# Optimization experiments

Measured on AMD Instinct MI355X. Metric: run time of the kernel, lower is better.

Reference implementation:

```python
import jax, jax.numpy as jnp
import numpy as np

S = 100        # sos_token_num
H = 12         # num heads
LY = 3         # number of residual blocks
NEG = -100.0   # attention-bias masking value


def layer_norm(x, w, b, eps=1e-5):
    u = jnp.mean(x, -1, keepdims=True)
    v = jnp.mean((x - u) ** 2, -1, keepdims=True)
    return (x - u) / jnp.sqrt(v + eps) * w + b


def quick_gelu(x):
    return x * jax.nn.sigmoid(1.702 * x)


def l2norm(x, eps=1e-12):
    return x / jnp.maximum(jnp.linalg.norm(x, axis=-1, keepdims=True), eps)


def setup_inputs() -> dict:
    key = jax.random.key(0)
    ks = iter(jax.random.split(key, 32))
    n, c, hh, ww, out_dim = 2, 768, 32, 32, 512
    r = lambda shape, s=1.0: jax.random.normal(next(ks), shape, jnp.float32) * s
    return dict(
        cls_token=r((1, n, c)),
        pix_feat=r((n, c, hh, ww)),
        last_surgery=r((1 + hh * ww, n, c)),
        attn_bias=r((n, 1, S, hh, ww)),
        qkv_w=r((LY, 3 * c, c), 0.02), qkv_b=jnp.zeros((LY, 3 * c)),
        proj_w=r((LY, c, c), 0.02), proj_b=jnp.zeros((LY, c)),
        ln1_w=jnp.ones((LY, c)), ln1_b=jnp.zeros((LY, c)),
        ln2_w=jnp.ones((LY, c)), ln2_b=jnp.zeros((LY, c)),
        fc_w=r((LY, 4 * c, c), 0.02), fc_b=jnp.zeros((LY, 4 * c)),
        fc2_w=r((LY, c, 4 * c), 0.02), fc2_b=jnp.zeros((LY, c)),
        lnp_w=jnp.ones((c,)), lnp_b=jnp.zeros((c,)),
        proj_out=r((c, out_dim), 0.02),
    )


def reference(cls_token, pix_feat, last_surgery, attn_bias,
              qkv_w, qkv_b, proj_w, proj_b,
              ln1_w, ln1_b, ln2_w, ln2_b,
              fc_w, fc_b, fc2_w, fc2_b,
              lnp_w, lnp_b, proj_out):
    n, c, hh, ww = pix_feat.shape
    L = hh * ww
    N = S + 1 + L
    d = c // H
    scale = d ** -0.5

    # ---- assemble token streams (batch-first [n, N, c]) ----
    pix_tok = pix_feat.reshape(n, c, L).transpose(2, 0, 1)          # [L, n, c]
    x = jnp.concatenate([jnp.broadcast_to(cls_token, (S, n, c)), cls_token, pix_tok], 0)
    x_sur = jnp.concatenate([jnp.broadcast_to(last_surgery[0:1], (S, n, c)), last_surgery], 0)
    xo = x.transpose(1, 0, 2)      # 'original' stream  [n, N, c]
    xs = x_sur.transpose(1, 0, 2)  # 'surgery'  stream  [n, N, c]

    # ---- build attention biases (identity downsample: bias already at (h, w)) ----
    base = jnp.zeros((N, N), jnp.float32)
    base = base.at[:, :S].set(NEG)
    base = base.at[jnp.arange(S), jnp.arange(S)].set(0.0)
    base = base.at[:S, S].set(NEG)
    plain = jnp.broadcast_to(base, (n, H, N, N))
    bias = jnp.broadcast_to(attn_bias, (n, H, S, hh, ww)).reshape(n, H, S, L)
    biased = plain.at[:, :, :S, S + 1:].set(bias)   # sos rows attend to pixels via bias

    def attention(t, l):
        # t: [n, N, c] (post-ln_1); returns (surgery_res, ori_res)
        qkv = (t @ qkv_w[l].T + qkv_b[l]).reshape(n, N, 3, H, d).transpose(2, 0, 3, 1, 4)
        q, k, v = qkv[0], qkv[1], qkv[2]   # each [n, H, N, d]
        def attend(q_, k_, mask):
            a = jax.nn.softmax(jnp.einsum('bhnd,bhmd->bhnm', q_, k_) * scale + mask, axis=-1)
            o = jnp.einsum('bhnm,bhmd->bhnd', a, v).transpose(0, 2, 1, 3).reshape(n, N, c)
            return o @ proj_w[l].T + proj_b[l]
        x_ori_res = attend(q, k, biased)   # standard pass, biased mask (attn_mask[0])
        x_res = attend(v, v, plain)        # q = k = v surgery pass (attn_mask[1])
        return x_res, x_ori_res

    for l in range(LY):
        t = layer_norm(xo, ln1_w[l], ln1_b[l])
        res_sur, res_ori = attention(t, l)
        xo = xo + res_ori
        xo = xo + (quick_gelu(layer_norm(xo, ln2_w[l], ln2_b[l]) @ fc_w[l].T + fc_b[l]) @ fc2_w[l].T + fc2_b[l])
        xs = xs + res_sur

    # ---- heads ----
    sos = l2norm(layer_norm(xo[:, :S], lnp_w, lnp_b) @ proj_out)          # [n, S, out]
    img = l2norm(layer_norm(xs[:, S:], lnp_w, lnp_b) @ proj_out)          # [n, 1+L, out]
    img = img[:, 1:, :].transpose(0, 2, 1).reshape(n, proj_out.shape[1], hh, ww)
    return sos, img
```

## Files before the change

### kernel.cpp

```cpp
#include <hip/hip_runtime.h>
#include <math.h>


constexpr int Cc = 768;
constexpr int Ss = 100;
constexpr int Hh = 12;
constexpr int Ll = 1024;
constexpr int Nn = 1125;
constexpr int NB = 2;
constexpr int VTS = 1216;
constexpr float QS = 0.18033688011112042f;
constexpr float LOG2E = 1.4426950408889634f;

typedef unsigned short u16;
typedef unsigned int u32;
typedef __attribute__((ext_vector_type(8))) short short8v;
typedef __attribute__((ext_vector_type(8))) unsigned short ushort8v;
typedef __attribute__((ext_vector_type(4))) float f32x4;
typedef __attribute__((ext_vector_type(4))) unsigned int u32x4;

__device__ inline u16 f2bf(float f) {
  unsigned u = __builtin_bit_cast(unsigned int, f);
  unsigned r = u + 0x7fffu + ((u >> 16) & 1u);
  return (u16)(r >> 16);
}
__device__ inline float bf2f(u16 v) {
  return __builtin_bit_cast(float, (unsigned int)v << 16);
}
__device__ inline unsigned cvtpk(float lo, float hi) {
  unsigned r;
  asm("v_cvt_pk_bf16_f32 %0, %1, %2" : "=v"(r) : "v"(lo), "v"(hi));
  return r;
}
__device__ inline float max3f(float a, float b, float c) {
  float r;
  asm("v_max3_f32 %0, %1, %2, %3" : "=v"(r) : "v"(a), "v"(b), "v"(c));
  return r;
}

__device__ inline int swz(int row, int col) {
  return (row << 6) + ((((col >> 3) ^ (row & 7)) << 3) | (col & 7));
}

__global__ __launch_bounds__(256) void assemble_kernel(
    const float* __restrict__ cls, const float* __restrict__ pix,
    const float* __restrict__ sur, float* __restrict__ xo, float* __restrict__ xs) {
  int idx = blockIdx.x * 256 + (int)threadIdx.x;
  int total = NB * Nn * Cc;
  if (idx >= total) return;
  int ch = idx % Cc;
  int t  = (idx / Cc) % Nn;
  int b  = idx / (Cc * Nn);
  float vo, vs;
  if (t <= Ss) vo = cls[b * Cc + ch];
  else         vo = pix[(size_t)b * Cc * Ll + (size_t)ch * Ll + (t - Ss - 1)];
  if (t < Ss)  vs = sur[b * Cc + ch];
  else         vs = sur[(size_t)(t - Ss) * NB * Cc + b * Cc + ch];
  xo[idx] = vo;
  xs[idx] = vs;
}

constexpr int CN0 = 3 * 2304 * 768;
constexpr int CN1 = 3 * 768 * 768;
constexpr int CN2 = 3 * 3072 * 768;
constexpr int CN3 = 3 * 768 * 3072;
__global__ __launch_bounds__(256) void cvt4_kernel(
    const float* __restrict__ s0, const float* __restrict__ s1,
    const float* __restrict__ s2, const float* __restrict__ s3,
    u16* __restrict__ dst) {
  int i4 = (blockIdx.x * 256 + (int)threadIdx.x) * 4;
  if (i4 >= CN0 + CN1 + CN2 + CN3) return;
  const float* src; int off;
  if (i4 < CN0)             { src = s0; off = i4; }
  else if (i4 < CN0 + CN1)  { src = s1; off = i4 - CN0; }
  else if (i4 < CN0 + CN1 + CN2) { src = s2; off = i4 - CN0 - CN1; }
  else                      { src = s3; off = i4 - CN0 - CN1 - CN2; }
  float4 v = *(const float4*)(src + off);
  *(ushort4*)(dst + i4) = make_ushort4(f2bf(v.x), f2bf(v.y), f2bf(v.z), f2bf(v.w));
}

__global__ __launch_bounds__(256) void transpose_po_kernel(
    const float* __restrict__ in, u16* __restrict__ out) {
  int id = blockIdx.x * 256 + (int)threadIdx.x;
  if (id >= 512 * 768) return;
  int nidx = id / 768, k = id - nidx * 768;
  out[id] = f2bf(in[(size_t)k * 512 + nidx]);
}

__global__ __launch_bounds__(256) void vtrans_kernel(
    const u16* __restrict__ qkv, u16* __restrict__ vtg) {
  __shared__ u16 tile[64][72];
  int tt = blockIdx.x;
  int bh = blockIdx.y;
  int b = bh / Hh, h = bh - b * Hh;
  int tid = (int)threadIdx.x;
  {
    int tl = tid >> 2, c0 = (tid & 3) << 4;
    int tok = tt * 64 + tl;
    int tokc = tok > 1124 ? 1124 : tok;
    const u16* src = qkv + ((size_t)(b * Nn + tokc)) * 2304 + 2 * Cc + h * 64 + c0;
    ushort8v v0 = *(const ushort8v*)src;
    ushort8v v1 = *(const ushort8v*)(src + 8);
    if (tok > 1124) { v0 = (ushort8v)0; v1 = (ushort8v)0; }
    *(ushort8v*)&tile[tl][c0] = v0;
    *(ushort8v*)&tile[tl][c0 + 8] = v1;
  }
  __syncthreads();
  {
    int d = tid >> 2, t0 = (tid & 3) << 4;
    ushort8v o0, o1;
#pragma unroll
    for (int j = 0; j < 8; ++j) { o0[j] = tile[t0 + j][d]; o1[j] = tile[t0 + 8 + j][d]; }
    size_t orow = ((size_t)bh * 64 + d) * VTS + tt * 64 + t0;
    *(ushort8v*)&vtg[orow] = o0;
    *(ushort8v*)&vtg[orow + 8] = o1;
  }
}

__global__ __launch_bounds__(256) void ln_kernel(
    const float* __restrict__ X, const float* __restrict__ w, const float* __restrict__ b,
    u16* __restrict__ Y, int rows_per_b, int row_off) {
  int r = blockIdx.x;
  int bb = r / rows_per_b;
  int i  = r % rows_per_b;
  const float* x = X + ((size_t)bb * Nn + row_off + i) * Cc;
  u16* y = Y + (size_t)r * Cc;
  int tid = (int)threadIdx.x;
  float v0 = x[tid], v1 = x[tid + 256], v2 = x[tid + 512];
  float s = v0 + v1 + v2;
  __shared__ float sbuf[4];
  for (int off = 32; off; off >>= 1) s += __shfl_xor(s, off);
  if ((tid & 63) == 0) sbuf[tid >> 6] = s;
  __syncthreads();
  float mean = (sbuf[0] + sbuf[1] + sbuf[2] + sbuf[3]) * (1.0f / Cc);
  float d0 = v0 - mean, d1 = v1 - mean, d2 = v2 - mean;
  float q = d0 * d0 + d1 * d1 + d2 * d2;
  __syncthreads();
  for (int off = 32; off; off >>= 1) q += __shfl_xor(q, off);
  if ((tid & 63) == 0) sbuf[tid >> 6] = q;
  __syncthreads();
  float var = (sbuf[0] + sbuf[1] + sbuf[2] + sbuf[3]) * (1.0f / Cc);
  float inv = rsqrtf(var + 1e-5f);
  y[tid]       = f2bf(d0 * inv * w[tid]       + b[tid]);
  y[tid + 256] = f2bf(d1 * inv * w[tid + 256] + b[tid + 256]);
  y[tid + 512] = f2bf(d2 * inv * w[tid + 512] + b[tid + 512]);
}

__global__ __launch_bounds__(256) void gemm64_kernel(
    const u16* __restrict__ A0, const u16* __restrict__ A1,
    const u16* __restrict__ B, const float* __restrict__ bias,
    const float* __restrict__ res0, const float* __restrict__ res1,
    float* __restrict__ outf0, float* __restrict__ outf1,
    u16* __restrict__ outb0, u16* __restrict__ outb1,
    int M, int N, int K, int act) {
  __shared__ __align__(16) u16 Als[64 * 64];
  __shared__ __align__(16) u16 Bls[128 * 64];
  int zz = blockIdx.z;
  const u16* A = zz ? A1 : A0;
  const float* res = zz ? res1 : res0;
  float* outf = zz ? outf1 : outf0;
  u16* outb = zz ? outb1 : outb0;
  int tid = (int)threadIdx.x;
  int wave = tid >> 6, lane = tid & 63, g = lane >> 4, li = lane & 15;
  int row0 = blockIdx.y * 64, col0 = blockIdx.x * 128;

  const u16* aptr[2]; int dA[2];
#pragma unroll
  for (int j = 0; j < 2; ++j) {
    int ca = tid + j * 256;
    int r = ca >> 3, c8 = ca & 7;
    dA[j] = (r << 6) + ((c8 ^ (r & 7)) << 3);
    int ra = row0 + r; if (ra > M - 1) ra = M - 1;
    aptr[j] = A + (size_t)ra * K + (c8 << 3);
  }
  const u16* bptr[4]; int dB[4];
#pragma unroll
  for (int j = 0; j < 4; ++j) {
    int cb = tid + j * 256;
    int r = cb >> 3, c8 = cb & 7;
    dB[j] = (r << 6) + ((c8 ^ (r & 7)) << 3);
    bptr[j] = B + (size_t)(col0 + r) * K + (c8 << 3);
  }

  f32x4 acc[4][2];
#pragma unroll
  for (int mi = 0; mi < 4; ++mi)
#pragma unroll
    for (int ni = 0; ni < 2; ++ni) acc[mi][ni] = (f32x4){0.f, 0.f, 0.f, 0.f};

  for (int k0 = 0; k0 < K; k0 += 64) {
    ushort8v ta[2], tb[4];
#pragma unroll
    for (int j = 0; j < 2; ++j) ta[j] = *(const ushort8v*)(aptr[j] + k0);
#pragma unroll
    for (int j = 0; j < 4; ++j) tb[j] = *(const ushort8v*)(bptr[j] + k0);
    __syncthreads();
#pragma unroll
    for (int j = 0; j < 2; ++j) *(ushort8v*)&Als[dA[j]] = ta[j];
#pragma unroll
    for (int j = 0; j < 4; ++j) *(ushort8v*)&Bls[dB[j]] = tb[j];
    __syncthreads();
#pragma unroll
    for (int kc = 0; kc < 2; ++kc) {
      short8v af[4], bfr[2];
#pragma unroll
      for (int mi = 0; mi < 4; ++mi) {
        int rr = mi * 16 + li;
        af[mi] = *(const short8v*)&Als[(rr << 6) + (((kc * 4 + g) ^ (rr & 7)) << 3)];
      }
#pragma unroll
      for (int ni = 0; ni < 2; ++ni) {
        int rb = wave * 32 + ni * 16 + li;
        bfr[ni] = *(const short8v*)&Bls[(rb << 6) + (((kc * 4 + g) ^ (rb & 7)) << 3)];
      }
      __builtin_amdgcn_s_setprio(1);
#pragma unroll
      for (int mi = 0; mi < 4; ++mi)
#pragma unroll
        for (int ni = 0; ni < 2; ++ni)
          acc[mi][ni] = __builtin_amdgcn_mfma_f32_16x16x32_bf16(af[mi], bfr[ni], acc[mi][ni], 0, 0, 0);
      __builtin_amdgcn_s_setprio(0);
    }
  }

#pragma unroll
  for (int mi = 0; mi < 4; ++mi) {
#pragma unroll
    for (int r = 0; r < 4; ++r) {
      int m = row0 + mi * 16 + g * 4 + r;
      if (m >= M) continue;
#pragma unroll
      for (int ni = 0; ni < 2; ++ni) {
        int n = col0 + wave * 32 + ni * 16 + li;
        float v = acc[mi][ni][r];
        if (bias) v += bias[n];
        if (act)  v = v / (1.0f + __expf(-1.702f * v));
        if (res)  v += res[(size_t)m * N + n];
        if (outf) outf[(size_t)m * N + n] = v;
        else      outb[(size_t)m * N + n] = f2bf(v);
      }
    }
  }
}

__global__ __launch_bounds__(256) void attn_kernel(
    const u16* __restrict__ qkv, const u16* __restrict__ vtg,
    const float* __restrict__ abias,
    u16* __restrict__ ao, u16* __restrict__ as_) {
  __shared__ __align__(16) u16 Klds[64 * 64];
  __shared__ __align__(16) u16 Vt[64 * 64];
  int id = (int)blockIdx.x;
  int virt = (id & 7) * 114 + (id >> 3);
  int gid = virt / 19;
  int qt  = virt - gid * 19;
  int z   = gid / 24;
  int bh  = gid - z * 24;
  int b = bh / Hh, h = bh - b * Hh;
  int tid = (int)threadIdx.x;
  int wave = tid >> 6, lane = tid & 63, g = lane >> 4, li = lane & 15;
  bool sosq = qt >= 17;
  u16* outp = z ? as_ : ao;

  int qbase = sosq ? (qt - 17) * 64 + wave * 16 : Ss + qt * 64 + wave * 16;
  int qtok = qbase + li;
  int qcap = sosq ? 99 : 1124;
  if (qtok > qcap) qtok = qcap;
  int qoff = z ? 2 * Cc + h * 64 : h * 64;
  int koff = z ? 2 * Cc + h * 64 : Cc + h * 64;

  short8v qf[2];
  {
    const u16* qp = qkv + ((size_t)b * Nn + qtok) * 2304 + qoff;
#pragma unroll
    for (int kc = 0; kc < 2; ++kc) {
      ushort8v a = *(const ushort8v*)(qp + kc * 32 + g * 8);
      u32x4 w;
#pragma unroll
      for (int jj = 0; jj < 4; ++jj)
        w[jj] = cvtpk(bf2f(a[2 * jj]) * QS, bf2f(a[2 * jj + 1]) * QS);
      qf[kc] = __builtin_bit_cast(short8v, w);
    }
  }

  int skey = tid >> 2;
  int sd0  = (tid & 3) << 4;
  int prow = 16 * (2 * (skey >> 5) + ((skey >> 2) & 1)) + 4 * ((skey >> 3) & 3) + (skey & 3);
  int kK0 = swz(prow, sd0), kK1 = swz(prow, sd0 + 8);
  int vI0 = swz(skey, sd0), vI1 = swz(skey, sd0 + 8);
  const u16* kbase = qkv + (size_t)b * Nn * 2304 + koff + sd0;
  const u16* vbase = vtg + ((size_t)bh * 64 + skey) * VTS + sd0;

  const int KOFF[4] = {0, 4, 32, 36};

  f32x4 oacc[4];
#pragma unroll
  for (int dt = 0; dt < 4; ++dt) oacc[dt] = (f32x4){0.f, 0.f, 0.f, 0.f};
  float mrow = -1e30f, lrow = 0.f;

  int NT = sosq ? 18 : 17;
  for (int kt = 0; kt < NT; ++kt) {
    int t0 = sosq ? (kt == 0 ? (qt - 17) * 64 : 64 * kt + 32) : 96 + 64 * kt;
    __syncthreads();
    {
      int ktok = t0 + skey; if (ktok > 1124) ktok = 1124;
      const u16* kp = kbase + (size_t)ktok * 2304;
      ushort8v k0v = *(const ushort8v*)kp;
      ushort8v k1v = *(const ushort8v*)(kp + 8);
      const u16* vp = vbase + t0;
      ushort8v v0 = *(const ushort8v*)vp;
      ushort8v v1 = *(const ushort8v*)(vp + 8);
      *(ushort8v*)&Klds[kK0] = k0v;
      *(ushort8v*)&Klds[kK1] = k1v;
      *(ushort8v*)&Vt[vI0] = v0;
      *(ushort8v*)&Vt[vI1] = v1;
    }
    __syncthreads();

    f32x4 sacc[4];
#pragma unroll
    for (int nt = 0; nt < 4; ++nt) sacc[nt] = (f32x4){0.f, 0.f, 0.f, 0.f};
    __builtin_amdgcn_s_setprio(1);
#pragma unroll
    for (int kc = 0; kc < 2; ++kc) {
#pragma unroll
      for (int nt = 0; nt < 4; ++nt) {
        short8v kb = *(const short8v*)&Klds[swz(nt * 16 + li, kc * 32 + g * 8)];
        sacc[nt] = __builtin_amdgcn_mfma_f32_16x16x32_bf16(kb, qf[kc], sacc[nt], 0, 0, 0);
      }
    }
    __builtin_amdgcn_s_setprio(0);

    int tg = t0 + 8 * g;
    if (!sosq) {
      if (kt == 0) {
#pragma unroll
        for (int nt = 0; nt < 4; ++nt)
#pragma unroll
          for (int r = 0; r < 4; ++r)
            if (tg + KOFF[nt] + r < 100) sacc[nt][r] = -1e30f;
      } else if (kt == 16) {
#pragma unroll
        for (int nt = 0; nt < 4; ++nt)
#pragma unroll
          for (int r = 0; r < 4; ++r)
            if (tg + KOFF[nt] + r > 1124) sacc[nt][r] = -1e30f;
      }
    } else {
      if (kt == 0) {
#pragma unroll
        for (int nt = 0; nt < 4; ++nt)
#pragma unroll
          for (int r = 0; r < 4; ++r)
            if (tg + KOFF[nt] + r != qtok) sacc[nt][r] = -1e30f;
      } else if (z == 0) {
        const float* bp = abias + ((size_t)b * Ss + qtok) * Ll;
#pragma unroll
        for (int nt = 0; nt < 4; ++nt)
#pragma unroll
          for (int r = 0; r < 4; ++r) {
            int tok = tg + KOFF[nt] + r;
            int bi = tok - 101; bi = bi < 0 ? 0 : bi; bi = bi > 1023 ? 1023 : bi;
            float bv = bp[bi];
            bool bad = (tok < 101) | (tok > 1124);
            sacc[nt][r] = bad ? -1e30f : fmaf(bv, LOG2E, sacc[nt][r]);
          }
      } else {
#pragma unroll
        for (int nt = 0; nt < 4; ++nt)
#pragma unroll
          for (int r = 0; r < 4; ++r) {
            int tok = tg + KOFF[nt] + r;
            if ((tok < 101) | (tok > 1124)) sacc[nt][r] = -1e30f;
          }
      }
    }

    float rmax = max3f(sacc[0][0], sacc[0][1], sacc[0][2]);
    rmax = max3f(rmax, sacc[0][3], sacc[1][0]);
    rmax = max3f(rmax, sacc[1][1], sacc[1][2]);
    rmax = max3f(rmax, sacc[1][3], sacc[2][0]);
    rmax = max3f(rmax, sacc[2][1], sacc[2][2]);
    rmax = max3f(rmax, sacc[2][3], sacc[3][0]);
    rmax = max3f(rmax, sacc[3][1], sacc[3][2]);
    rmax = fmaxf(rmax, sacc[3][3]);
    rmax = fmaxf(rmax, __shfl_xor(rmax, 16));
    rmax = fmaxf(rmax, __shfl_xor(rmax, 32));
    float mnew = fmaxf(mrow, rmax);
    float fac = __builtin_amdgcn_exp2f(mrow - mnew);
    mrow = mnew;
    float psum = 0.f;
#pragma unroll
    for (int nt = 0; nt < 4; ++nt)
#pragma unroll
      for (int r = 0; r < 4; ++r) {
        float e = __builtin_amdgcn_exp2f(sacc[nt][r] - mnew);
        sacc[nt][r] = e;
        psum += e;
      }
    psum += __shfl_xor(psum, 16);
    psum += __shfl_xor(psum, 32);
    lrow = lrow * fac + psum;
#pragma unroll
    for (int dt = 0; dt < 4; ++dt) oacc[dt] *= fac;

    __builtin_amdgcn_s_setprio(1);
#pragma unroll
    for (int kcp = 0; kcp < 2; ++kcp) {
      u32x4 pwv;
#pragma unroll
      for (int w = 0; w < 4; ++w) {
        int nt = 2 * kcp + (w >> 1);
        int r0 = (w & 1) * 2;
        pwv[w] = cvtpk(sacc[nt][r0], sacc[nt][r0 + 1]);
      }
      short8v pb = __builtin_bit_cast(short8v, pwv);
#pragma unroll
      for (int dt = 0; dt < 4; ++dt) {
        short8v va = *(const short8v*)&Vt[swz(dt * 16 + li, kcp * 32 + g * 8)];
        oacc[dt] = __builtin_amdgcn_mfma_f32_16x16x32_bf16(va, pb, oacc[dt], 0, 0, 0);
      }
    }
    __builtin_amdgcn_s_setprio(0);
  }

  int tok = qbase + li;
  if (tok <= qcap) {
    float inv = 1.0f / lrow;
    u16* op = outp + ((size_t)b * Nn + tok) * Cc + h * 64 + g * 4;
#pragma unroll
    for (int dt = 0; dt < 4; ++dt) {
      unsigned lo = cvtpk(oacc[dt][0] * inv, oacc[dt][1] * inv);
      unsigned hi = cvtpk(oacc[dt][2] * inv, oacc[dt][3] * inv);
      uint2 o2; o2.x = lo; o2.y = hi;
      *(uint2*)(op + dt * 16) = o2;
    }
  }
}

__global__ __launch_bounds__(256) void l2norm_sos_kernel(
    const float* __restrict__ Xp, float* __restrict__ out) {
  int r = blockIdx.x;
  int tid = (int)threadIdx.x;
  const float* x = Xp + (size_t)r * 512;
  float v0 = x[tid], v1 = x[tid + 256];
  float s = v0 * v0 + v1 * v1;
  __shared__ float sbuf[4];
  for (int off = 32; off; off >>= 1) s += __shfl_xor(s, off);
  if ((tid & 63) == 0) sbuf[tid >> 6] = s;
  __syncthreads();
  float tot = sbuf[0] + sbuf[1] + sbuf[2] + sbuf[3];
  float inv = 1.0f / fmaxf(sqrtf(tot), 1e-12f);
  out[(size_t)r * 512 + tid]       = v0 * inv;
  out[(size_t)r * 512 + tid + 256] = v1 * inv;
}

__global__ __launch_bounds__(256) void l2norm_img_kernel(
    const float* __restrict__ Xp, float* __restrict__ out) {
  int r = blockIdx.x;
  int b = r / 1025, ti = r % 1025;
  int tid = (int)threadIdx.x;
  const float* x = Xp + (size_t)r * 512;
  float v0 = x[tid], v1 = x[tid + 256];
  float s = v0 * v0 + v1 * v1;
  __shared__ float sbuf[4];
  for (int off = 32; off; off >>= 1) s += __shfl_xor(s, off);
  if ((tid & 63) == 0) sbuf[tid >> 6] = s;
  __syncthreads();
  float tot = sbuf[0] + sbuf[1] + sbuf[2] + sbuf[3];
  if (ti == 0) return;
  float inv = 1.0f / fmaxf(sqrtf(tot), 1e-12f);
  float* o = out + (size_t)b * 512 * 1024 + (ti - 1);
  o[(size_t)tid * 1024]         = v0 * inv;
  o[(size_t)(tid + 256) * 1024] = v1 * inv;
}

extern "C" void kernel_launch(void* const* d_in, const int* in_sizes, int n_in,
                              void* d_out, int out_size, void* d_ws, size_t ws_size,
                              hipStream_t stream) {
  const float* cls      = (const float*)d_in[0];
  const float* pix      = (const float*)d_in[1];
  const float* sur      = (const float*)d_in[2];
  const float* abias    = (const float*)d_in[3];
  const float* qkv_w    = (const float*)d_in[4];
  const float* qkv_b    = (const float*)d_in[5];
  const float* proj_w   = (const float*)d_in[6];
  const float* proj_b   = (const float*)d_in[7];
  const float* ln1_w    = (const float*)d_in[8];
  const float* ln1_b    = (const float*)d_in[9];
  const float* ln2_w    = (const float*)d_in[10];
  const float* ln2_b    = (const float*)d_in[11];
  const float* fc_w     = (const float*)d_in[12];
  const float* fc_b     = (const float*)d_in[13];
  const float* fc2_w    = (const float*)d_in[14];
  const float* fc2_b    = (const float*)d_in[15];
  const float* lnp_w    = (const float*)d_in[16];
  const float* lnp_b    = (const float*)d_in[17];
  const float* proj_o   = (const float*)d_in[18];
  float* out = (float*)d_out;

  const size_t SZ = (size_t)NB * Nn * Cc;
  float* xo      = (float*)d_ws;
  float* xs      = xo + SZ;
  float* head_pj = xs + SZ;
  u16* tln_bf = (u16*)(head_pj + 2250 * 512);
  u16* act_bf = tln_bf + (size_t)2250 * 768;
  u16* ao_bf  = act_bf + (size_t)2250 * 3072;
  u16* as_bf  = ao_bf + (size_t)2250 * 768;
  u16* wq_bf  = as_bf + (size_t)2250 * 768;
  u16* wp_bf  = wq_bf + (size_t)CN0;
  u16* wf_bf  = wp_bf + (size_t)CN1;
  u16* w2_bf  = wf_bf + (size_t)CN2;
  u16* wo_bf  = w2_bf + (size_t)CN3;
  u16* vtg    = wo_bf + (size_t)512 * 768;

  assemble_kernel<<<6750, 256, 0, stream>>>(cls, pix, sur, xo, xs);
  cvt4_kernel<<<20736, 256, 0, stream>>>(qkv_w, proj_w, fc_w, fc2_w, wq_bf);
  transpose_po_kernel<<<1536, 256, 0, stream>>>(proj_o, wo_bf);

  for (int l = 0; l < 3; ++l) {
    ln_kernel<<<2250, 256, 0, stream>>>(xo, ln1_w + l * 768, ln1_b + l * 768, tln_bf, Nn, 0);
    gemm64_kernel<<<dim3(18, 36, 1), 256, 0, stream>>>(
        tln_bf, tln_bf, wq_bf + (size_t)l * 2304 * 768, qkv_b + l * 2304,
        nullptr, nullptr, nullptr, nullptr, act_bf, act_bf, 2250, 2304, 768, 0);
    vtrans_kernel<<<dim3(19, 24), 256, 0, stream>>>(act_bf, vtg);
    attn_kernel<<<912, 256, 0, stream>>>(act_bf, vtg, abias, ao_bf, as_bf);
    gemm64_kernel<<<dim3(6, 36, 2), 256, 0, stream>>>(
        ao_bf, as_bf, wp_bf + (size_t)l * 768 * 768, proj_b + l * 768,
        xo, xs, xo, xs, nullptr, nullptr, 2250, 768, 768, 0);
    ln_kernel<<<2250, 256, 0, stream>>>(xo, ln2_w + l * 768, ln2_b + l * 768, tln_bf, Nn, 0);
    gemm64_kernel<<<dim3(24, 36, 1), 256, 0, stream>>>(
        tln_bf, tln_bf, wf_bf + (size_t)l * 3072 * 768, fc_b + l * 3072,
        nullptr, nullptr, nullptr, nullptr, act_bf, act_bf, 2250, 3072, 768, 1);
    gemm64_kernel<<<dim3(6, 36, 1), 256, 0, stream>>>(
        act_bf, act_bf, w2_bf + (size_t)l * 768 * 3072, fc2_b + l * 768,
        xo, xo, xo, xo, nullptr, nullptr, 2250, 768, 3072, 0);
  }

  ln_kernel<<<200, 256, 0, stream>>>(xo, lnp_w, lnp_b, tln_bf, 100, 0);
  ln_kernel<<<2050, 256, 0, stream>>>(xs, lnp_w, lnp_b, tln_bf + 200 * 768, 1025, 100);
  gemm64_kernel<<<dim3(4, 36, 1), 256, 0, stream>>>(
      tln_bf, tln_bf, wo_bf, nullptr,
      nullptr, nullptr, head_pj, head_pj, nullptr, nullptr, 2250, 512, 768, 0);
  l2norm_sos_kernel<<<200, 256, 0, stream>>>(head_pj, out);
  l2norm_img_kernel<<<2050, 256, 0, stream>>>(head_pj + 200 * 512, out + 102400);
}
```

Baseline: 754.8 us.

## Add 128x128 GEMM for QKV/FC and process two query fragments per attention wave

Adds a gemm128 kernel that uses 128x128 tiles with 4x4 MFMA fragments per wave, and routes the QKV and FC1 GEMMs through it. Larger tiles raise arithmetic intensity and reuse of the loaded A and B tiles. The attention kernel now handles 32 query rows per wave (128 per block) instead of 16, so each K/V tile loaded into LDS is reused across twice as many queries. The SOS query tile is restructured to cover all 100 SOS queries in one block. In exchange, register pressure goes up and the grids shrink, which can lower occupancy and leave CUs underused.

```diff
diff --git a/kernel.cpp b/kernel.cpp
--- a/kernel.cpp
+++ b/kernel.cpp
@@ -146,6 +146,89 @@
   y[tid + 512] = f2bf(d2 * inv * w[tid + 512] + b[tid + 512]);
 }
 
+__global__ __launch_bounds__(256) void gemm128_kernel(
+    const u16* __restrict__ A, const u16* __restrict__ B,
+    const float* __restrict__ bias, u16* __restrict__ outb,
+    int M, int N, int K, int act) {
+  __shared__ __align__(16) u16 Als[128 * 64];
+  __shared__ __align__(16) u16 Bls[128 * 64];
+  int tid = (int)threadIdx.x;
+  int wave = tid >> 6, lane = tid & 63, g = lane >> 4, li = lane & 15;
+  int wm = wave >> 1, wn = wave & 1;
+  int row0 = blockIdx.y * 128, col0 = blockIdx.x * 128;
+
+  const u16* aptr[4]; const u16* bptr[4]; int dsti[4];
+#pragma unroll
+  for (int j = 0; j < 4; ++j) {
+    int c = tid + j * 256;
+    int r = c >> 3, c8 = c & 7;
+    dsti[j] = (r << 6) + ((c8 ^ (r & 7)) << 3);
+    int ra = row0 + r; if (ra > M - 1) ra = M - 1;
+    aptr[j] = A + (size_t)ra * K + (c8 << 3);
+    bptr[j] = B + (size_t)(col0 + r) * K + (c8 << 3);
+  }
+
+  f32x4 acc[4][4];
+#pragma unroll
+  for (int mi = 0; mi < 4; ++mi)
+#pragma unroll
+    for (int ni = 0; ni < 4; ++ni) acc[mi][ni] = (f32x4){0.f, 0.f, 0.f, 0.f};
+
+  for (int k0 = 0; k0 < K; k0 += 64) {
+    ushort8v ta[4], tb[4];
+#pragma unroll
+    for (int j = 0; j < 4; ++j) {
+      ta[j] = *(const ushort8v*)(aptr[j] + k0);
+      tb[j] = *(const ushort8v*)(bptr[j] + k0);
+    }
+    __syncthreads();
+#pragma unroll
+    for (int j = 0; j < 4; ++j) {
+      *(ushort8v*)&Als[dsti[j]] = ta[j];
+      *(ushort8v*)&Bls[dsti[j]] = tb[j];
+    }
+    __syncthreads();
+#pragma unroll
+    for (int kc = 0; kc < 2; ++kc) {
+      short8v af[4], bfr[4];
+#pragma unroll
+      for (int mi = 0; mi < 4; ++mi) {
+        int rr = wm * 64 + mi * 16 + li;
+        af[mi] = *(const short8v*)&Als[(rr << 6) + (((kc * 4 + g) ^ (rr & 7)) << 3)];
+      }
+#pragma unroll
+      for (int ni = 0; ni < 4; ++ni) {
+        int rb = wn * 64 + ni * 16 + li;
+        bfr[ni] = *(const short8v*)&Bls[(rb << 6) + (((kc * 4 + g) ^ (rb & 7)) << 3)];
+      }
+      __builtin_amdgcn_s_setprio(1);
+#pragma unroll
+      for (int mi = 0; mi < 4; ++mi)
+#pragma unroll
+        for (int ni = 0; ni < 4; ++ni)
+          acc[mi][ni] = __builtin_amdgcn_mfma_f32_16x16x32_bf16(af[mi], bfr[ni], acc[mi][ni], 0, 0, 0);
+      __builtin_amdgcn_s_setprio(0);
+    }
+  }
+
+#pragma unroll
+  for (int mi = 0; mi < 4; ++mi) {
+#pragma unroll
+    for (int r = 0; r < 4; ++r) {
+      int m = row0 + wm * 64 + mi * 16 + g * 4 + r;
+      if (m >= M) continue;
+#pragma unroll
+      for (int ni = 0; ni < 4; ++ni) {
+        int n = col0 + wn * 64 + ni * 16 + li;
+        float v = acc[mi][ni][r];
+        if (bias) v += bias[n];
+        if (act)  v = v / (1.0f + __expf(-1.702f * v));
+        outb[(size_t)m * N + n] = f2bf(v);
+      }
+    }
+  }
+}
+
 __global__ __launch_bounds__(256) void gemm64_kernel(
     const u16* __restrict__ A0, const u16* __restrict__ A1,
     const u16* __restrict__ B, const float* __restrict__ bias,
@@ -250,27 +333,29 @@
   __shared__ __align__(16) u16 Klds[64 * 64];
   __shared__ __align__(16) u16 Vt[64 * 64];
   int id = (int)blockIdx.x;
-  int virt = (id & 7) * 114 + (id >> 3);
-  int gid = virt / 19;
-  int qt  = virt - gid * 19;
+  int virt = (id & 7) * 60 + (id >> 3);
+  int gid = virt / 10;
+  int qt  = virt - gid * 10;
   int z   = gid / 24;
   int bh  = gid - z * 24;
   int b = bh / Hh, h = bh - b * Hh;
   int tid = (int)threadIdx.x;
   int wave = tid >> 6, lane = tid & 63, g = lane >> 4, li = lane & 15;
-  bool sosq = qt >= 17;
+  bool sosq = (qt == 9);
   u16* outp = z ? as_ : ao;
 
-  int qbase = sosq ? (qt - 17) * 64 + wave * 16 : Ss + qt * 64 + wave * 16;
-  int qtok = qbase + li;
+  int qbase = sosq ? wave * 32 : 100 + qt * 128 + wave * 32;
   int qcap = sosq ? 99 : 1124;
-  if (qtok > qcap) qtok = qcap;
+  int qtokf[2];
+  qtokf[0] = qbase + li;       if (qtokf[0] > qcap) qtokf[0] = qcap;
+  qtokf[1] = qbase + 16 + li;  if (qtokf[1] > qcap) qtokf[1] = qcap;
   int qoff = z ? 2 * Cc + h * 64 : h * 64;
   int koff = z ? 2 * Cc + h * 64 : Cc + h * 64;
 
-  short8v qf[2];
-  {
-    const u16* qp = qkv + ((size_t)b * Nn + qtok) * 2304 + qoff;
+  short8v qf[2][2];
+#pragma unroll
+  for (int f = 0; f < 2; ++f) {
+    const u16* qp = qkv + ((size_t)b * Nn + qtokf[f]) * 2304 + qoff;
 #pragma unroll
     for (int kc = 0; kc < 2; ++kc) {
       ushort8v a = *(const ushort8v*)(qp + kc * 32 + g * 8);
@@ -278,7 +363,7 @@
 #pragma unroll
       for (int jj = 0; jj < 4; ++jj)
         w[jj] = cvtpk(bf2f(a[2 * jj]) * QS, bf2f(a[2 * jj + 1]) * QS);
-      qf[kc] = __builtin_bit_cast(short8v, w);
+      qf[f][kc] = __builtin_bit_cast(short8v, w);
     }
   }
 
@@ -292,14 +377,16 @@
 
   const int KOFF[4] = {0, 4, 32, 36};
 
-  f32x4 oacc[4];
-#pragma unroll
-  for (int dt = 0; dt < 4; ++dt) oacc[dt] = (f32x4){0.f, 0.f, 0.f, 0.f};
-  float mrow = -1e30f, lrow = 0.f;
-
-  int NT = sosq ? 18 : 17;
+  f32x4 oacc[2][4];
+#pragma unroll
+  for (int f = 0; f < 2; ++f)
+#pragma unroll
+    for (int dt = 0; dt < 4; ++dt) oacc[f][dt] = (f32x4){0.f, 0.f, 0.f, 0.f};
+  float mrow[2] = {-1e30f, -1e30f}, lrow[2] = {0.f, 0.f};
+
+  int NT = sosq ? 19 : 17;
   for (int kt = 0; kt < NT; ++kt) {
-    int t0 = sosq ? (kt == 0 ? (qt - 17) * 64 : 64 * kt + 32) : 96 + 64 * kt;
+    int t0 = sosq ? (kt <= 1 ? 64 * kt : 64 * (kt - 1) + 32) : 96 + 64 * kt;
     __syncthreads();
     {
       int ktok = t0 + skey; if (ktok > 1124) ktok = 1124;
@@ -316,16 +403,19 @@
     }
     __syncthreads();
 
-    f32x4 sacc[4];
-#pragma unroll
-    for (int nt = 0; nt < 4; ++nt) sacc[nt] = (f32x4){0.f, 0.f, 0.f, 0.f};
+    f32x4 sacc[2][4];
+#pragma unroll
+    for (int f = 0; f < 2; ++f)
+#pragma unroll
+      for (int nt = 0; nt < 4; ++nt) sacc[f][nt] = (f32x4){0.f, 0.f, 0.f, 0.f};
     __builtin_amdgcn_s_setprio(1);
 #pragma unroll
     for (int kc = 0; kc < 2; ++kc) {
 #pragma unroll
       for (int nt = 0; nt < 4; ++nt) {
         short8v kb = *(const short8v*)&Klds[swz(nt * 16 + li, kc * 32 + g * 8)];
-        sacc[nt] = __builtin_amdgcn_mfma_f32_16x16x32_bf16(kb, qf[kc], sacc[nt], 0, 0, 0);
+        sacc[0][nt] = __builtin_amdgcn_mfma_f32_16x16x32_bf16(kb, qf[0][kc], sacc[0][nt], 0, 0, 0);
+        sacc[1][nt] = __builtin_amdgcn_mfma_f32_16x16x32_bf16(kb, qf[1][kc], sacc[1][nt], 0, 0, 0);
       }
     }
     __builtin_amdgcn_s_setprio(0);
@@ -334,103 +424,124 @@
     if (!sosq) {
       if (kt == 0) {
 #pragma unroll
-        for (int nt = 0; nt < 4; ++nt)
-#pragma unroll
-          for (int r = 0; r < 4; ++r)
-            if (tg + KOFF[nt] + r < 100) sacc[nt][r] = -1e30f;
+        for (int f = 0; f < 2; ++f)
+#pragma unroll
+          for (int nt = 0; nt < 4; ++nt)
+#pragma unroll
+            for (int r = 0; r < 4; ++r)
+              if (tg + KOFF[nt] + r < 100) sacc[f][nt][r] = -1e30f;
       } else if (kt == 16) {
 #pragma unroll
-        for (int nt = 0; nt < 4; ++nt)
-#pragma unroll
-          for (int r = 0; r < 4; ++r)
-            if (tg + KOFF[nt] + r > 1124) sacc[nt][r] = -1e30f;
+        for (int f = 0; f < 2; ++f)
+#pragma unroll
+          for (int nt = 0; nt < 4; ++nt)
+#pragma unroll
+            for (int r = 0; r < 4; ++r)
+              if (tg + KOFF[nt] + r > 1124) sacc[f][nt][r] = -1e30f;
       }
     } else {
-      if (kt == 0) {
-#pragma unroll
-        for (int nt = 0; nt < 4; ++nt)
-#pragma unroll
-          for (int r = 0; r < 4; ++r)
-            if (tg + KOFF[nt] + r != qtok) sacc[nt][r] = -1e30f;
+      if (kt <= 1) {
+#pragma unroll
+        for (int f = 0; f < 2; ++f)
+#pragma unroll
+          for (int nt = 0; nt < 4; ++nt)
+#pragma unroll
+            for (int r = 0; r < 4; ++r)
+              if (tg + KOFF[nt] + r != qtokf[f]) sacc[f][nt][r] = -1e30f;
       } else if (z == 0) {
-        const float* bp = abias + ((size_t)b * Ss + qtok) * Ll;
-#pragma unroll
-        for (int nt = 0; nt < 4; ++nt)
-#pragma unroll
-          for (int r = 0; r < 4; ++r) {
-            int tok = tg + KOFF[nt] + r;
-            int bi = tok - 101; bi = bi < 0 ? 0 : bi; bi = bi > 1023 ? 1023 : bi;
-            float bv = bp[bi];
-            bool bad = (tok < 101) | (tok > 1124);
-            sacc[nt][r] = bad ? -1e30f : fmaf(bv, LOG2E, sacc[nt][r]);
-          }
+#pragma unroll
+        for (int f = 0; f < 2; ++f) {
+          const float* bp = abias + ((size_t)b * Ss + qtokf[f]) * Ll;
+#pragma unroll
+          for (int nt = 0; nt < 4; ++nt)
+#pragma unroll
+            for (int r = 0; r < 4; ++r) {
+              int tok = tg + KOFF[nt] + r;
+              int bi = tok - 101; bi = bi < 0 ? 0 : bi; bi = bi > 1023 ? 1023 : bi;
+              float bv = bp[bi];
+              bool bad = (tok < 101) | (tok > 1124);
+              sacc[f][nt][r] = bad ? -1e30f : fmaf(bv, LOG2E, sacc[f][nt][r]);
+            }
+        }
       } else {
 #pragma unroll
-        for (int nt = 0; nt < 4; ++nt)
-#pragma unroll
-          for (int r = 0; r < 4; ++r) {
-            int tok = tg + KOFF[nt] + r;
-            if ((tok < 101) | (tok > 1124)) sacc[nt][r] = -1e30f;
-          }
-      }
-    }
-
-    float rmax = max3f(sacc[0][0], sacc[0][1], sacc[0][2]);
-    rmax = max3f(rmax, sacc[0][3], sacc[1][0]);
-    rmax = max3f(rmax, sacc[1][1], sacc[1][2]);
-    rmax = max3f(rmax, sacc[1][3], sacc[2][0]);
-    rmax = max3f(rmax, sacc[2][1], sacc[2][2]);
-    rmax = max3f(rmax, sacc[2][3], sacc[3][0]);
-    rmax = max3f(rmax, sacc[3][1], sacc[3][2]);
-    rmax = fmaxf(rmax, sacc[3][3]);
-    rmax = fmaxf(rmax, __shfl_xor(rmax, 16));
-    rmax = fmaxf(rmax, __shfl_xor(rmax, 32));
-    float mnew = fmaxf(mrow, rmax);
-    float fac = __builtin_amdgcn_exp2f(mrow - mnew);
-    mrow = mnew;
-    float psum = 0.f;
-#pragma unroll
-    for (int nt = 0; nt < 4; ++nt)
-#pragma unroll
-      for (int r = 0; r < 4; ++r) {
-        float e = __builtin_amdgcn_exp2f(sacc[nt][r] - mnew);
-        sacc[nt][r] = e;
-        psum += e;
-      }
-    psum += __shfl_xor(psum, 16);
-    psum += __shfl_xor(psum, 32);
-    lrow = lrow * fac + psum;
-#pragma unroll
-    for (int dt = 0; dt < 4; ++dt) oacc[dt] *= fac;
+        for (int f = 0; f < 2; ++f)
+#pragma unroll
+          for (int nt = 0; nt < 4; ++nt)
+#pragma unroll
+            for (int r = 0; r < 4; ++r) {
+              int tok = tg + KOFF[nt] + r;
+              if ((tok < 101) | (tok > 1124)) sacc[f][nt][r] = -1e30f;
+            }
+      }
+    }
+
+#pragma unroll
+    for (int f = 0; f < 2; ++f) {
+      float rmax = max3f(sacc[f][0][0], sacc[f][0][1], sacc[f][0][2]);
+      rmax = max3f(rmax, sacc[f][0][3], sacc[f][1][0]);
+      rmax = max3f(rmax, sacc[f][1][1], sacc[f][1][2]);
+      rmax = max3f(rmax, sacc[f][1][3], sacc[f][2][0]);
+      rmax = max3f(rmax, sacc[f][2][1], sacc[f][2][2]);
+      rmax = max3f(rmax, sacc[f][2][3], sacc[f][3][0]);
+      rmax = max3f(rmax, sacc[f][3][1], sacc[f][3][2]);
+      rmax = fmaxf(rmax, sacc[f][3][3]);
+      rmax = fmaxf(rmax, __shfl_xor(rmax, 16));
+      rmax = fmaxf(rmax, __shfl_xor(rmax, 32));
+      float mnew = fmaxf(mrow[f], rmax);
+      float fac = __builtin_amdgcn_exp2f(mrow[f] - mnew);
+      mrow[f] = mnew;
+      float psum = 0.f;
+#pragma unroll
+      for (int nt = 0; nt < 4; ++nt)
+#pragma unroll
+        for (int r = 0; r < 4; ++r) {
+          float e = __builtin_amdgcn_exp2f(sacc[f][nt][r] - mnew);
+          sacc[f][nt][r] = e;
+          psum += e;
+        }
+      psum += __shfl_xor(psum, 16);
+      psum += __shfl_xor(psum, 32);
+      lrow[f] = lrow[f] * fac + psum;
+#pragma unroll
+      for (int dt = 0; dt < 4; ++dt) oacc[f][dt] *= fac;
+    }
 
     __builtin_amdgcn_s_setprio(1);
 #pragma unroll
     for (int kcp = 0; kcp < 2; ++kcp) {
-      u32x4 pwv;
-#pragma unroll
-      for (int w = 0; w < 4; ++w) {
-        int nt = 2 * kcp + (w >> 1);
-        int r0 = (w & 1) * 2;
-        pwv[w] = cvtpk(sacc[nt][r0], sacc[nt][r0 + 1]);
-      }
-      short8v pb = __builtin_bit_cast(short8v, pwv);
+      short8v pb[2];
+#pragma unroll
+      for (int f = 0; f < 2; ++f) {
+        u32x4 pwv;
+#pragma unroll
+        for (int w = 0; w < 4; ++w) {
+          int nt = 2 * kcp + (w >> 1);
+          int r0 = (w & 1) * 2;
+          pwv[w] = cvtpk(sacc[f][nt][r0], sacc[f][nt][r0 + 1]);
+        }
+        pb[f] = __builtin_bit_cast(short8v, pwv);
+      }
 #pragma unroll
       for (int dt = 0; dt < 4; ++dt) {
         short8v va = *(const short8v*)&Vt[swz(dt * 16 + li, kcp * 32 + g * 8)];
-        oacc[dt] = __builtin_amdgcn_mfma_f32_16x16x32_bf16(va, pb, oacc[dt], 0, 0, 0);
+        oacc[0][dt] = __builtin_amdgcn_mfma_f32_16x16x32_bf16(va, pb[0], oacc[0][dt], 0, 0, 0);
+        oacc[1][dt] = __builtin_amdgcn_mfma_f32_16x16x32_bf16(va, pb[1], oacc[1][dt], 0, 0, 0);
       }
     }
     __builtin_amdgcn_s_setprio(0);
   }
 
-  int tok = qbase + li;
-  if (tok <= qcap) {
-    float inv = 1.0f / lrow;
+#pragma unroll
+  for (int f = 0; f < 2; ++f) {
+    int tok = qbase + f * 16 + li;
+    if (tok > qcap) continue;
+    float inv = 1.0f / lrow[f];
     u16* op = outp + ((size_t)b * Nn + tok) * Cc + h * 64 + g * 4;
 #pragma unroll
     for (int dt = 0; dt < 4; ++dt) {
-      unsigned lo = cvtpk(oacc[dt][0] * inv, oacc[dt][1] * inv);
-      unsigned hi = cvtpk(oacc[dt][2] * inv, oacc[dt][3] * inv);
+      unsigned lo = cvtpk(oacc[f][dt][0] * inv, oacc[f][dt][1] * inv);
+      unsigned hi = cvtpk(oacc[f][dt][2] * inv, oacc[f][dt][3] * inv);
       uint2 o2; o2.x = lo; o2.y = hi;
       *(uint2*)(op + dt * 16) = o2;
     }
@@ -519,18 +630,18 @@
 
   for (int l = 0; l < 3; ++l) {
     ln_kernel<<<2250, 256, 0, stream>>>(xo, ln1_w + l * 768, ln1_b + l * 768, tln_bf, Nn, 0);
-    gemm64_kernel<<<dim3(18, 36, 1), 256, 0, stream>>>(
-        tln_bf, tln_bf, wq_bf + (size_t)l * 2304 * 768, qkv_b + l * 2304,
-        nullptr, nullptr, nullptr, nullptr, act_bf, act_bf, 2250, 2304, 768, 0);
+    gemm128_kernel<<<dim3(18, 18), 256, 0, stream>>>(
+        tln_bf, wq_bf + (size_t)l * 2304 * 768, qkv_b + l * 2304,
+        act_bf, 2250, 2304, 768, 0);
     vtrans_kernel<<<dim3(19, 24), 256, 0, stream>>>(act_bf, vtg);
-    attn_kernel<<<912, 256, 0, stream>>>(act_bf, vtg, abias, ao_bf, as_bf);
+    attn_kernel<<<480, 256, 0, stream>>>(act_bf, vtg, abias, ao_bf, as_bf);
     gemm64_kernel<<<dim3(6, 36, 2), 256, 0, stream>>>(
         ao_bf, as_bf, wp_bf + (size_t)l * 768 * 768, proj_b + l * 768,
         xo, xs, xo, xs, nullptr, nullptr, 2250, 768, 768, 0);
     ln_kernel<<<2250, 256, 0, stream>>>(xo, ln2_w + l * 768, ln2_b + l * 768, tln_bf, Nn, 0);
-    gemm64_kernel<<<dim3(24, 36, 1), 256, 0, stream>>>(
-        tln_bf, tln_bf, wf_bf + (size_t)l * 3072 * 768, fc_b + l * 3072,
-        nullptr, nullptr, nullptr, nullptr, act_bf, act_bf, 2250, 3072, 768, 1);
+    gemm128_kernel<<<dim3(24, 18), 256, 0, stream>>>(
+        tln_bf, wf_bf + (size_t)l * 3072 * 768, fc_b + l * 3072,
+        act_bf, 2250, 3072, 768, 1);
     gemm64_kernel<<<dim3(6, 36, 1), 256, 0, stream>>>(
         act_bf, act_bf, w2_bf + (size_t)l * 768 * 3072, fc2_b + l * 768,
         xo, xo, xo, xo, nullptr, nullptr, 2250, 768, 3072, 0);
```

Result: slower. 837.2 us (+10.9%).
